# Performance work log

Measured on AMD Instinct MI355X. Metric: run time of the kernel, lower is better.

## Reference

```python
import jax, jax.numpy as jnp
import numpy as np

WS = 8      # window_size
SS = 4      # shift_size
NH = 16     # num_heads


def _rel_position_index(ws):
    # matches WindowMSA.double_step_seq + flip(1)
    seq1 = np.arange(0, (2 * ws - 1) * ws, 2 * ws - 1)
    seq2 = np.arange(0, ws)
    rel = (seq1[:, None] + seq2[None, :]).reshape(1, -1)  # (1, ws*ws)
    idx = rel + rel.T                                      # (ws*ws, ws*ws)
    return np.ascontiguousarray(idx[:, ::-1]).astype(np.int32)


def _shift_attn_mask(H, W, ws, ss):
    # static numpy construction of the Swin shift mask, (nW, N, N)
    img = np.zeros((H, W), dtype=np.int32)
    slices = (slice(0, -ws), slice(-ws, -ss), slice(-ss, None))
    cnt = 0
    for h in slices:
        for w in slices:
            img[h, w] = cnt
            cnt += 1
    win = img.reshape(H // ws, ws, W // ws, ws).transpose(0, 2, 1, 3).reshape(-1, ws * ws)
    diff = win[:, None, :] - win[:, :, None]
    return np.where(diff != 0, -100.0, 0.0).astype(np.float32)


def setup_inputs() -> dict:
    key = jax.random.key(0)
    ks = jax.random.split(key, 6)
    B, H, W, C = 16, 64, 64, 512
    return {
        "query": jax.random.normal(ks[0], (B, H * W, C), jnp.float32),
        "qkv_w": jax.random.normal(ks[1], (3 * C, C), jnp.float32) * 0.02,
        "qkv_b": jnp.zeros((3 * C,), jnp.float32),
        "proj_w": jax.random.normal(ks[2], (C, C), jnp.float32) * 0.02,
        "proj_b": jnp.zeros((C,), jnp.float32),
        "bias_table": jax.random.normal(ks[3], ((2 * WS - 1) ** 2, NH), jnp.float32) * 0.02,
        "rel_index": jnp.asarray(_rel_position_index(WS)),
        "H": H,
        "W": W,
    }


def reference(query, qkv_w, qkv_b, proj_w, proj_b, bias_table, rel_index, H, W):
    B, L, C = query.shape
    hd = C // NH
    scale = hd ** -0.5
    N = WS * WS
    nW = (H // WS) * (W // WS)

    x = query.reshape(B, H, W, C)
    # cyclic shift
    x = jnp.roll(x, (-SS, -SS), axis=(1, 2))
    # window partition -> (B*nW, N, C)
    xw = x.reshape(B, H // WS, WS, W // WS, WS, C).transpose(0, 1, 3, 2, 4, 5)
    xw = xw.reshape(B * nW, N, C)

    # qkv projection
    qkv = xw @ qkv_w.T + qkv_b                       # (BnW, N, 3C)
    qkv = qkv.reshape(B * nW, N, 3, NH, hd).transpose(2, 0, 3, 1, 4)
    q, k, v = qkv[0], qkv[1], qkv[2]                 # (BnW, NH, N, hd)

    attn = jnp.einsum('whnd,whmd->whnm', q * scale, k)

    # relative position bias (N, N, NH) -> (NH, N, N)
    bias = bias_table[rel_index.reshape(-1)].reshape(N, N, NH).transpose(2, 0, 1)
    attn = attn + bias[None]

    # shift mask (static)
    mask = jnp.asarray(_shift_attn_mask(H, W, WS, SS))  # (nW, N, N)
    attn = attn.reshape(B, nW, NH, N, N) + mask[None, :, None]
    attn = jax.nn.softmax(attn.reshape(B * nW, NH, N, N), axis=-1)

    out = jnp.einsum('whnm,whmd->whnd', attn, v)     # (BnW, NH, N, hd)
    out = out.transpose(0, 2, 1, 3).reshape(B * nW, N, C)
    out = out @ proj_w.T + proj_b

    # window reverse -> (B, H, W, C)
    out = out.reshape(B, H // WS, W // WS, WS, WS, C).transpose(0, 1, 3, 2, 4, 5)
    out = out.reshape(B, H, W, C)
    # reverse cyclic shift
    out = jnp.roll(out, (SS, SS), axis=(1, 2))
    return out.reshape(B, H * W, C)
```

## Files before the change

kernel.cpp:

```cpp
#include <hip/hip_runtime.h>


typedef short  short8  __attribute__((ext_vector_type(8)));
typedef short  short4v __attribute__((ext_vector_type(4)));
typedef float  floatx4 __attribute__((ext_vector_type(4)));

#define DEVI static __device__ __forceinline__

DEVI unsigned short f2bf(float f) {
    union { float f; unsigned int u; } v;
    v.f = f;
    return (unsigned short)((v.u + 0x7fffu + ((v.u >> 16) & 1u)) >> 16);
}

__global__ void cvt_all(const float* __restrict__ query,
                        const float* __restrict__ qkv_w,
                        const float* __restrict__ proj_w,
                        unsigned short* __restrict__ wbf,
                        unsigned short* __restrict__ xw) {
    const int bid = blockIdx.x;
    if (bid < 1024) {
        const int idx = ((bid << 8) + threadIdx.x) << 2;
        const float* src = (idx < 786432) ? (qkv_w + idx) : (proj_w + (idx - 786432));
        const floatx4 v = *(const floatx4*)src;
        short4v o;
        o[0] = (short)f2bf(v[0]); o[1] = (short)f2bf(v[1]);
        o[2] = (short)f2bf(v[2]); o[3] = (short)f2bf(v[3]);
        *(short4v*)(wbf + idx) = o;
        return;
    }
    const int c   = ((bid - 1024) << 8) + threadIdx.x;
    const int win = c >> 12;
    const int rem = c & 4095;
    const int jc  = rem & 3;
    const int tok = (rem >> 2) & 63;
    const int kc  = rem >> 8;
    const int b   = win >> 6, wy = (win >> 3) & 7, wx = win & 7;
    const int ty  = tok >> 3, tx = tok & 7;
    const int gh  = ((wy << 3) + ty + 4) & 63;
    const int gw  = ((wx << 3) + tx + 4) & 63;
    const float* src = query + (((b << 12) + (gh << 6) + gw) << 9) + (kc << 5) + (jc << 3);
    const floatx4 v0 = *(const floatx4*)src;
    const floatx4 v1 = *(const floatx4*)(src + 4);
    short8 s;
    s[0] = (short)f2bf(v0[0]); s[1] = (short)f2bf(v0[1]);
    s[2] = (short)f2bf(v0[2]); s[3] = (short)f2bf(v0[3]);
    s[4] = (short)f2bf(v1[0]); s[5] = (short)f2bf(v1[1]);
    s[6] = (short)f2bf(v1[2]); s[7] = (short)f2bf(v1[3]);
    *(short8*)(xw + (win << 15) + (kc << 11) + (tok << 5) + (jc << 3)) = s;
}

template<int GX>
__global__ __launch_bounds__(256, GX ? 2 : 1)
void k_fused(const float* __restrict__ query,
             const unsigned short* __restrict__ wbf,
             const unsigned short* __restrict__ xw,
             const float* __restrict__ qkv_b,
             const float* __restrict__ proj_b,
             const float* __restrict__ bias_table,
             float* __restrict__ out)
{
    __shared__ __align__(16) unsigned short smem[GX ? 33280 : 62976];

    const int tid  = threadIdx.x;
    const int lane = tid & 63;
    const int l15  = lane & 15;
    const int quad = lane >> 4;
    const int wave = tid >> 6;

    const int win = blockIdx.x;
    const int b   = win >> 6;
    const int wy  = (win >> 3) & 7;
    const int wx  = win & 7;
    const int mid = ((wy == 7) ? 2 : 0) | ((wx == 7) ? 1 : 0);

    unsigned short* xs  = smem;
    unsigned short* wb  = smem + (GX ? 0 : 33280) + wave * 7424;
    unsigned short* qbf = wb;
    unsigned short* kbf = wb + 2560;
    unsigned short* vT  = wb + 5120;
    unsigned short* pbf = wb;

    if constexpr (!GX) {
        #pragma unroll
        for (int it = 0; it < 32; ++it) {
            const int c   = tid + (it << 8);
            const int tok = c >> 7;
            const int fo  = (c & 127) << 2;
            const int ty  = tok >> 3, tx = tok & 7;
            const int gh  = ((wy << 3) + ty + 4) & 63;
            const int gw  = ((wx << 3) + tx + 4) & 63;
            const floatx4 v = *(const floatx4*)(query + (((b << 12) + (gh << 6) + gw) << 9) + fo);
            short4v s;
            s[0] = (short)f2bf(v[0]); s[1] = (short)f2bf(v[1]);
            s[2] = (short)f2bf(v[2]); s[3] = (short)f2bf(v[3]);
            *(short4v*)&xs[tok * 520 + fo] = s;
        }
        __syncthreads();
    }

    const unsigned short* xa = xw + (win << 15) + (l15 << 5) + (quad << 3);

    const float scale = 0.17677669529663687f;
    const floatx4 fz = {0.f, 0.f, 0.f, 0.f};

    unsigned int po[4][16];

    for (int hh = 0; hh < 4; ++hh) {
        const int h = (wave << 2) + hh;

        floatx4 accq[4][2], acck[4][2], accv[4][2];
        #pragma unroll
        for (int mt = 0; mt < 4; ++mt)
            #pragma unroll
            for (int nt = 0; nt < 2; ++nt) { accq[mt][nt] = fz; acck[mt][nt] = fz; accv[mt][nt] = fz; }

        const unsigned short* wq = wbf + ((h << 5) + l15) * 512 + (quad << 3);
        const unsigned short* wk = wq + 512 * 512;
        const unsigned short* wv = wk + 512 * 512;

        #pragma unroll 2
        for (int kk = 0; kk < 512; kk += 32) {
            short8 a[4], bq[2], bk2[2], bv2[2];
            #pragma unroll
            for (int mt = 0; mt < 4; ++mt) {
                if constexpr (GX)
                    a[mt] = *(const short8*)(xa + (kk << 6) + (mt << 9));
                else
                    a[mt] = *(const short8*)&xs[((mt << 4) + l15) * 520 + kk + (quad << 3)];
            }
            #pragma unroll
            for (int nt = 0; nt < 2; ++nt) {
                const int ro = (nt << 4) * 512 + kk;
                bq[nt]  = *(const short8*)(wq + ro);
                bk2[nt] = *(const short8*)(wk + ro);
                bv2[nt] = *(const short8*)(wv + ro);
            }
            #pragma unroll
            for (int nt = 0; nt < 2; ++nt)
                #pragma unroll
                for (int mt = 0; mt < 4; ++mt) {
                    accq[mt][nt] = __builtin_amdgcn_mfma_f32_16x16x32_bf16(a[mt], bq[nt],  accq[mt][nt], 0, 0, 0);
                    acck[mt][nt] = __builtin_amdgcn_mfma_f32_16x16x32_bf16(a[mt], bk2[nt], acck[mt][nt], 0, 0, 0);
                    accv[mt][nt] = __builtin_amdgcn_mfma_f32_16x16x32_bf16(a[mt], bv2[nt], accv[mt][nt], 0, 0, 0);
                }
        }

        #pragma unroll
        for (int nt = 0; nt < 2; ++nt) {
            const int cix = (h << 5) + (nt << 4) + l15;
            const float bq_ = qkv_b[cix];
            const float bk_ = qkv_b[512 + cix];
            const float bv_ = qkv_b[1024 + cix];
            #pragma unroll
            for (int mt = 0; mt < 4; ++mt) {
                short4v vv;
                #pragma unroll
                for (int r = 0; r < 4; ++r) {
                    const int row = (mt << 4) + (quad << 2) + r;
                    qbf[row * 40 + (nt << 4) + l15] = f2bf(accq[mt][nt][r] + bq_);
                    kbf[row * 40 + (nt << 4) + l15] = f2bf(acck[mt][nt][r] + bk_);
                    vv[r] = (short)f2bf(accv[mt][nt][r] + bv_);
                }
                *(short4v*)&vT[((nt << 4) + l15) * 72 + (mt << 4) + (quad << 2)] = vv;
            }
        }

        short8 qa[4], ka[4];
        #pragma unroll
        for (int t = 0; t < 4; ++t) {
            qa[t] = *(const short8*)&qbf[((t << 4) + l15) * 40 + (quad << 3)];
            ka[t] = *(const short8*)&kbf[((t << 4) + l15) * 40 + (quad << 3)];
        }
        floatx4 s4[4][4];
        #pragma unroll
        for (int mt = 0; mt < 4; ++mt)
            #pragma unroll
            for (int nt = 0; nt < 4; ++nt)
                s4[mt][nt] = __builtin_amdgcn_mfma_f32_16x16x32_bf16(qa[mt], ka[nt], fz, 0, 0, 0);

        int  gjv[4]; bool jrow[4], jcol[4];
        #pragma unroll
        for (int nt = 0; nt < 4; ++nt) {
            const int j  = (nt << 4) + l15;
            const int j2 = 63 - j;
            gjv[nt]  = 15 * (j2 >> 3) + (j2 & 7);
            jrow[nt] = (j >> 3) < 4;
            jcol[nt] = (j & 7) < 4;
        }
        #pragma unroll
        for (int mt = 0; mt < 4; ++mt) {
            const int i0  = (mt << 4) + (quad << 2);
            const int fi0 = 15 * (i0 >> 3) + (i0 & 7);
            const bool irow = (i0 >> 3) < 4;
            const bool icol = (i0 & 7) == 0;
            #pragma unroll
            for (int nt = 0; nt < 4; ++nt) {
                float mval = 0.0f;
                if ((mid & 2) && (irow != jrow[nt])) mval = -100.0f;
                if ((mid & 1) && (icol != jcol[nt])) mval = -100.0f;
                const float* bp = bias_table + (fi0 + gjv[nt]) * 16 + h;
                #pragma unroll
                for (int r = 0; r < 4; ++r)
                    s4[mt][nt][r] = s4[mt][nt][r] * scale + bp[r * 16] + mval;
            }
        }

        #pragma unroll
        for (int mt = 0; mt < 4; ++mt)
            #pragma unroll
            for (int r = 0; r < 4; ++r) {
                float m = fmaxf(fmaxf(s4[mt][0][r], s4[mt][1][r]),
                                fmaxf(s4[mt][2][r], s4[mt][3][r]));
                m = fmaxf(m, __shfl_xor(m, 1));
                m = fmaxf(m, __shfl_xor(m, 2));
                m = fmaxf(m, __shfl_xor(m, 4));
                m = fmaxf(m, __shfl_xor(m, 8));
                float loc = 0.0f;
                #pragma unroll
                for (int nt = 0; nt < 4; ++nt) {
                    s4[mt][nt][r] = __expf(s4[mt][nt][r] - m);
                    loc += s4[mt][nt][r];
                }
                loc += __shfl_xor(loc, 1);
                loc += __shfl_xor(loc, 2);
                loc += __shfl_xor(loc, 4);
                loc += __shfl_xor(loc, 8);
                const float inv = 1.0f / loc;
                const int row = (mt << 4) + (quad << 2) + r;
                #pragma unroll
                for (int nt = 0; nt < 4; ++nt)
                    pbf[row * 72 + (nt << 4) + l15] = f2bf(s4[mt][nt][r] * inv);
            }

        short8 pa[4][2], va[2][2];
        #pragma unroll
        for (int mt = 0; mt < 4; ++mt)
            #pragma unroll
            for (int ks = 0; ks < 2; ++ks)
                pa[mt][ks] = *(const short8*)&pbf[((mt << 4) + l15) * 72 + (ks << 5) + (quad << 3)];
        #pragma unroll
        for (int nt = 0; nt < 2; ++nt)
            #pragma unroll
            for (int ks = 0; ks < 2; ++ks)
                va[nt][ks] = *(const short8*)&vT[((nt << 4) + l15) * 72 + (ks << 5) + (quad << 3)];

        #pragma unroll
        for (int mt = 0; mt < 4; ++mt)
            #pragma unroll
            for (int nt = 0; nt < 2; ++nt) {
                floatx4 acc = fz;
                acc = __builtin_amdgcn_mfma_f32_16x16x32_bf16(pa[mt][0], va[nt][0], acc, 0, 0, 0);
                acc = __builtin_amdgcn_mfma_f32_16x16x32_bf16(pa[mt][1], va[nt][1], acc, 0, 0, 0);
                const int pi = ((mt << 1) + nt) << 1;
                po[hh][pi]     = (unsigned int)f2bf(acc[0]) | ((unsigned int)f2bf(acc[1]) << 16);
                po[hh][pi + 1] = (unsigned int)f2bf(acc[2]) | ((unsigned int)f2bf(acc[3]) << 16);
            }
    }
    __syncthreads();

    #pragma unroll
    for (int hh = 0; hh < 4; ++hh) {
        const int ch0 = (((wave << 2) + hh) << 5) + l15;
        #pragma unroll
        for (int mt = 0; mt < 4; ++mt)
            #pragma unroll
            for (int nt = 0; nt < 2; ++nt) {
                const int pi = ((mt << 1) + nt) << 1;
                #pragma unroll
                for (int r = 0; r < 4; ++r) {
                    const int row = (mt << 4) + (quad << 2) + r;
                    const unsigned int w = po[hh][pi + (r >> 1)];
                    xs[row * 520 + ch0 + (nt << 4)] =
                        (unsigned short)((w >> ((r & 1) << 4)) & 0xffffu);
                }
            }
    }
    __syncthreads();

    const unsigned short* pwb = wbf + 786432;
    for (int pass = 0; pass < 2; ++pass) {
        const int co0 = (wave << 7) + (pass << 6);
        floatx4 acc[4][4];
        #pragma unroll
        for (int mt = 0; mt < 4; ++mt)
            #pragma unroll
            for (int nt = 0; nt < 4; ++nt) acc[mt][nt] = fz;

        const unsigned short* wp = pwb + (co0 + l15) * 512 + (quad << 3);

        #pragma unroll 2
        for (int kk = 0; kk < 512; kk += 32) {
            short8 a[4], bfr[4];
            #pragma unroll
            for (int mt = 0; mt < 4; ++mt)
                a[mt] = *(const short8*)&xs[((mt << 4) + l15) * 520 + kk + (quad << 3)];
            #pragma unroll
            for (int nt = 0; nt < 4; ++nt)
                bfr[nt] = *(const short8*)(wp + (nt << 4) * 512 + kk);
            #pragma unroll
            for (int nt = 0; nt < 4; ++nt)
                #pragma unroll
                for (int mt = 0; mt < 4; ++mt)
                    acc[mt][nt] = __builtin_amdgcn_mfma_f32_16x16x32_bf16(a[mt], bfr[nt], acc[mt][nt], 0, 0, 0);
        }

        #pragma unroll
        for (int nt = 0; nt < 4; ++nt) {
            const float pb_ = proj_b[co0 + (nt << 4) + l15];
            #pragma unroll
            for (int mt = 0; mt < 4; ++mt)
                #pragma unroll
                for (int r = 0; r < 4; ++r) {
                    const int tok = (mt << 4) + (quad << 2) + r;
                    const int ty = tok >> 3, tx = tok & 7;
                    const int gh = ((wy << 3) + ty + 4) & 63;
                    const int gw = ((wx << 3) + tx + 4) & 63;
                    out[(((b << 12) + (gh << 6) + gw) << 9) + co0 + (nt << 4) + l15] =
                        acc[mt][nt][r] + pb_;
                }
        }
    }
}

extern "C" void kernel_launch(void* const* d_in, const int* in_sizes, int n_in,
                              void* d_out, int out_size, void* d_ws, size_t ws_size,
                              hipStream_t stream) {
    const float* query      = (const float*)d_in[0];
    const float* qkv_w      = (const float*)d_in[1];
    const float* qkv_b      = (const float*)d_in[2];
    const float* proj_w     = (const float*)d_in[3];
    const float* proj_b     = (const float*)d_in[4];
    const float* bias_table = (const float*)d_in[5];

    unsigned short* wbf = (unsigned short*)d_ws;
    unsigned short* xw  = wbf + 1048576;

    const size_t need = (size_t)(1048576 + 33554432) * sizeof(unsigned short);
    if (ws_size >= need) {
        hipLaunchKernelGGL(cvt_all, dim3(17408), dim3(256), 0, stream,
                           query, qkv_w, proj_w, wbf, xw);
        hipLaunchKernelGGL(HIP_KERNEL_NAME(k_fused<1>), dim3(1024), dim3(256), 0, stream,
                           query, wbf, xw, qkv_b, proj_b, bias_table, (float*)d_out);
    } else {
        hipLaunchKernelGGL(cvt_all, dim3(1024), dim3(256), 0, stream,
                           query, qkv_w, proj_w, wbf, wbf);
        hipLaunchKernelGGL(HIP_KERNEL_NAME(k_fused<0>), dim3(1024), dim3(256), 0, stream,
                           query, wbf, wbf, qkv_b, proj_b, bias_table, (float*)d_out);
    }
}
```

Measured before the change: 409.1 us.

## Split fused window attention into separate attention and projection kernels

The fused kernel is split into two. k_attn computes QKV, softmax and PV for each window and writes the bf16 attention output back into the xw buffer in place. k_proj then runs the output projection and un-shifted scatter as its own kernel with higher occupancy. k_attn now uses a smaller, XOR-swizzled per-wave LDS layout so three blocks can fit per CU. The cost is an extra launch plus a bf16 round trip of the attention output through global memory.

```diff
diff --git a/kernel.cpp b/kernel.cpp
--- a/kernel.cpp
+++ b/kernel.cpp
@@ -50,17 +50,13 @@
     *(short8*)(xw + (win << 15) + (kc << 11) + (tok << 5) + (jc << 3)) = s;
 }
 
-template<int GX>
-__global__ __launch_bounds__(256, GX ? 2 : 1)
-void k_fused(const float* __restrict__ query,
-             const unsigned short* __restrict__ wbf,
-             const unsigned short* __restrict__ xw,
-             const float* __restrict__ qkv_b,
-             const float* __restrict__ proj_b,
-             const float* __restrict__ bias_table,
-             float* __restrict__ out)
+__global__ __launch_bounds__(256, 3)
+void k_attn(const unsigned short* __restrict__ wbf,
+            unsigned short* __restrict__ xw,
+            const float* __restrict__ qkv_b,
+            const float* __restrict__ bias_table)
 {
-    __shared__ __align__(16) unsigned short smem[GX ? 33280 : 62976];
+    __shared__ __align__(16) unsigned short smem[24576];
 
     const int tid  = threadIdx.x;
     const int lane = tid & 63;
@@ -69,46 +65,321 @@
     const int wave = tid >> 6;
 
     const int win = blockIdx.x;
+    const int wy  = (win >> 3) & 7;
+    const int wx  = win & 7;
+    const int mid = ((wy == 7) ? 2 : 0) | ((wx == 7) ? 1 : 0);
+
+    unsigned short* wbs = smem + wave * 6144;
+    unsigned short* qbf = wbs;
+    unsigned short* kbf = wbs + 2048;
+    unsigned short* vT  = wbs + 4096;
+    unsigned short* pbf = wbs;
+
+    const int sw4 = (l15 & 3) ^ (l15 >> 2);
+    const int sw8 = (l15 & 7) ^ (l15 >> 3);
+
+    const unsigned short* xa = xw + (win << 15) + (l15 << 5) + (quad << 3);
+
+    const float scale = 0.17677669529663687f;
+    const floatx4 fz = {0.f, 0.f, 0.f, 0.f};
+
+    unsigned int po[4][16];
+
+    for (int hh = 0; hh < 4; ++hh) {
+        const int h = (wave << 2) + hh;
+
+        floatx4 accq[4][2], acck[4][2], accv[4][2];
+        #pragma unroll
+        for (int mt = 0; mt < 4; ++mt)
+            #pragma unroll
+            for (int nt = 0; nt < 2; ++nt) { accq[mt][nt] = fz; acck[mt][nt] = fz; accv[mt][nt] = fz; }
+
+        const unsigned short* wq = wbf + ((h << 5) + l15) * 512 + (quad << 3);
+        const unsigned short* wk = wq + 512 * 512;
+        const unsigned short* wv = wk + 512 * 512;
+
+        #pragma unroll 2
+        for (int kk = 0; kk < 512; kk += 32) {
+            short8 a[4], bq[2], bk2[2], bv2[2];
+            #pragma unroll
+            for (int mt = 0; mt < 4; ++mt)
+                a[mt] = *(const short8*)(xa + (kk << 6) + (mt << 9));
+            #pragma unroll
+            for (int nt = 0; nt < 2; ++nt) {
+                const int ro = (nt << 4) * 512 + kk;
+                bq[nt]  = *(const short8*)(wq + ro);
+                bk2[nt] = *(const short8*)(wk + ro);
+                bv2[nt] = *(const short8*)(wv + ro);
+            }
+            #pragma unroll
+            for (int nt = 0; nt < 2; ++nt)
+                #pragma unroll
+                for (int mt = 0; mt < 4; ++mt) {
+                    accq[mt][nt] = __builtin_amdgcn_mfma_f32_16x16x32_bf16(a[mt], bq[nt],  accq[mt][nt], 0, 0, 0);
+                    acck[mt][nt] = __builtin_amdgcn_mfma_f32_16x16x32_bf16(a[mt], bk2[nt], acck[mt][nt], 0, 0, 0);
+                    accv[mt][nt] = __builtin_amdgcn_mfma_f32_16x16x32_bf16(a[mt], bv2[nt], accv[mt][nt], 0, 0, 0);
+                }
+        }
+
+        #pragma unroll
+        for (int nt = 0; nt < 2; ++nt) {
+            const int cix = (h << 5) + (nt << 4) + l15;
+            const float bq_ = qkv_b[cix];
+            const float bk_ = qkv_b[512 + cix];
+            const float bv_ = qkv_b[1024 + cix];
+            #pragma unroll
+            for (int mt = 0; mt < 4; ++mt) {
+                short4v vv;
+                #pragma unroll
+                for (int r = 0; r < 4; ++r) {
+                    const int row = (mt << 4) + (quad << 2) + r;
+                    const int ph  = (2 * nt + (l15 >> 3)) ^ (row & 3) ^ ((row >> 2) & 3);
+                    const int off = (row << 5) + (l15 & 7) + (ph << 3);
+                    qbf[off] = f2bf(accq[mt][nt][r] + bq_);
+                    kbf[off] = f2bf(acck[mt][nt][r] + bk_);
+                    vv[r] = (short)f2bf(accv[mt][nt][r] + bv_);
+                }
+                const int vph = (2 * mt + (quad >> 1)) ^ sw8;
+                *(short4v*)&vT[(((nt << 4) + l15) << 6) + ((quad & 1) << 2) + (vph << 3)] = vv;
+            }
+        }
+
+        short8 qa[4], ka[4];
+        #pragma unroll
+        for (int t = 0; t < 4; ++t) {
+            const int off = ((((t << 4) + l15)) << 5) + ((quad ^ sw4) << 3);
+            qa[t] = *(const short8*)&qbf[off];
+            ka[t] = *(const short8*)&kbf[off];
+        }
+        floatx4 s4[4][4];
+        #pragma unroll
+        for (int mt = 0; mt < 4; ++mt)
+            #pragma unroll
+            for (int nt = 0; nt < 4; ++nt)
+                s4[mt][nt] = __builtin_amdgcn_mfma_f32_16x16x32_bf16(qa[mt], ka[nt], fz, 0, 0, 0);
+
+        int  gjv[4]; bool jrow[4], jcol[4];
+        #pragma unroll
+        for (int nt = 0; nt < 4; ++nt) {
+            const int j  = (nt << 4) + l15;
+            const int j2 = 63 - j;
+            gjv[nt]  = 15 * (j2 >> 3) + (j2 & 7);
+            jrow[nt] = (j >> 3) < 4;
+            jcol[nt] = (j & 7) < 4;
+        }
+        #pragma unroll
+        for (int mt = 0; mt < 4; ++mt) {
+            const int i0  = (mt << 4) + (quad << 2);
+            const int fi0 = 15 * (i0 >> 3) + (i0 & 7);
+            const bool irow = (i0 >> 3) < 4;
+            const bool icol = (i0 & 7) == 0;
+            #pragma unroll
+            for (int nt = 0; nt < 4; ++nt) {
+                float mval = 0.0f;
+                if ((mid & 2) && (irow != jrow[nt])) mval = -100.0f;
+                if ((mid & 1) && (icol != jcol[nt])) mval = -100.0f;
+                const float* bp = bias_table + (fi0 + gjv[nt]) * 16 + h;
+                #pragma unroll
+                for (int r = 0; r < 4; ++r)
+                    s4[mt][nt][r] = s4[mt][nt][r] * scale + bp[r * 16] + mval;
+            }
+        }
+
+        float linv[4][4];
+        #pragma unroll
+        for (int mt = 0; mt < 4; ++mt)
+            #pragma unroll
+            for (int r = 0; r < 4; ++r) {
+                float m = fmaxf(fmaxf(s4[mt][0][r], s4[mt][1][r]),
+                                fmaxf(s4[mt][2][r], s4[mt][3][r]));
+                m = fmaxf(m, __shfl_xor(m, 1));
+                m = fmaxf(m, __shfl_xor(m, 2));
+                m = fmaxf(m, __shfl_xor(m, 4));
+                m = fmaxf(m, __shfl_xor(m, 8));
+                float loc = 0.0f;
+                #pragma unroll
+                for (int nt = 0; nt < 4; ++nt) {
+                    s4[mt][nt][r] = __expf(s4[mt][nt][r] - m);
+                    loc += s4[mt][nt][r];
+                }
+                loc += __shfl_xor(loc, 1);
+                loc += __shfl_xor(loc, 2);
+                loc += __shfl_xor(loc, 4);
+                loc += __shfl_xor(loc, 8);
+                linv[mt][r] = 1.0f / loc;
+                const int row = (mt << 4) + (quad << 2) + r;
+                #pragma unroll
+                for (int nt = 0; nt < 4; ++nt) {
+                    const int ph = (2 * nt + (l15 >> 3)) ^ (row & 7) ^ ((row >> 3) & 1);
+                    pbf[(row << 6) + (l15 & 7) + (ph << 3)] = f2bf(s4[mt][nt][r]);
+                }
+            }
+
+        short8 pa[4][2], va[2][2];
+        #pragma unroll
+        for (int mt = 0; mt < 4; ++mt)
+            #pragma unroll
+            for (int ks = 0; ks < 2; ++ks)
+                pa[mt][ks] = *(const short8*)&pbf[((((mt << 4) + l15)) << 6) + ((((ks << 2) + quad) ^ sw8) << 3)];
+        #pragma unroll
+        for (int nt = 0; nt < 2; ++nt)
+            #pragma unroll
+            for (int ks = 0; ks < 2; ++ks)
+                va[nt][ks] = *(const short8*)&vT[((((nt << 4) + l15)) << 6) + ((((ks << 2) + quad) ^ sw8) << 3)];
+
+        #pragma unroll
+        for (int mt = 0; mt < 4; ++mt)
+            #pragma unroll
+            for (int nt = 0; nt < 2; ++nt) {
+                floatx4 acc = fz;
+                acc = __builtin_amdgcn_mfma_f32_16x16x32_bf16(pa[mt][0], va[nt][0], acc, 0, 0, 0);
+                acc = __builtin_amdgcn_mfma_f32_16x16x32_bf16(pa[mt][1], va[nt][1], acc, 0, 0, 0);
+                const int pi = ((mt << 1) + nt) << 1;
+                po[hh][pi]     = (unsigned int)f2bf(acc[0] * linv[mt][0]) |
+                                 ((unsigned int)f2bf(acc[1] * linv[mt][1]) << 16);
+                po[hh][pi + 1] = (unsigned int)f2bf(acc[2] * linv[mt][2]) |
+                                 ((unsigned int)f2bf(acc[3] * linv[mt][3]) << 16);
+            }
+    }
+
+    __syncthreads();
+
+    unsigned short* yw = xw + (win << 15);
+    #pragma unroll
+    for (int hh = 0; hh < 4; ++hh) {
+        const int kcb = ((wave << 2) + hh) << 11;
+        #pragma unroll
+        for (int mt = 0; mt < 4; ++mt)
+            #pragma unroll
+            for (int nt = 0; nt < 2; ++nt) {
+                const int pi = ((mt << 1) + nt) << 1;
+                #pragma unroll
+                for (int r = 0; r < 4; ++r) {
+                    const int tok = (mt << 4) + (quad << 2) + r;
+                    const unsigned int w = po[hh][pi + (r >> 1)];
+                    yw[kcb + (tok << 5) + (nt << 4) + l15] =
+                        (unsigned short)((w >> ((r & 1) << 4)) & 0xffffu);
+                }
+            }
+    }
+}
+
+__global__ __launch_bounds__(256, 4)
+void k_proj(const unsigned short* __restrict__ wbf,
+            const unsigned short* __restrict__ yw,
+            const float* __restrict__ proj_b,
+            float* __restrict__ out)
+{
+    const int tid  = threadIdx.x;
+    const int lane = tid & 63;
+    const int l15  = lane & 15;
+    const int quad = lane >> 4;
+    const int wave = tid >> 6;
+
+    const int win = blockIdx.x;
+    const int b   = win >> 6;
+    const int wy  = (win >> 3) & 7;
+    const int wx  = win & 7;
+
+    const unsigned short* ya  = yw + (win << 15) + (l15 << 5) + (quad << 3);
+    const unsigned short* pwb = wbf + 786432;
+    const floatx4 fz = {0.f, 0.f, 0.f, 0.f};
+
+    for (int pass = 0; pass < 2; ++pass) {
+        const int co0 = (wave << 7) + (pass << 6);
+        floatx4 acc[4][4];
+        #pragma unroll
+        for (int mt = 0; mt < 4; ++mt)
+            #pragma unroll
+            for (int nt = 0; nt < 4; ++nt) acc[mt][nt] = fz;
+
+        const unsigned short* wp = pwb + (co0 + l15) * 512 + (quad << 3);
+
+        #pragma unroll 2
+        for (int kk = 0; kk < 512; kk += 32) {
+            short8 a[4], bfr[4];
+            #pragma unroll
+            for (int mt = 0; mt < 4; ++mt)
+                a[mt] = *(const short8*)(ya + (kk << 6) + (mt << 9));
+            #pragma unroll
+            for (int nt = 0; nt < 4; ++nt)
+                bfr[nt] = *(const short8*)(wp + (nt << 4) * 512 + kk);
+            #pragma unroll
+            for (int nt = 0; nt < 4; ++nt)
+                #pragma unroll
+                for (int mt = 0; mt < 4; ++mt)
+                    acc[mt][nt] = __builtin_amdgcn_mfma_f32_16x16x32_bf16(a[mt], bfr[nt], acc[mt][nt], 0, 0, 0);
+        }
+
+        #pragma unroll
+        for (int nt = 0; nt < 4; ++nt) {
+            const float pb_ = proj_b[co0 + (nt << 4) + l15];
+            #pragma unroll
+            for (int mt = 0; mt < 4; ++mt)
+                #pragma unroll
+                for (int r = 0; r < 4; ++r) {
+                    const int tok = (mt << 4) + (quad << 2) + r;
+                    const int ty = tok >> 3, tx = tok & 7;
+                    const int gh = ((wy << 3) + ty + 4) & 63;
+                    const int gw = ((wx << 3) + tx + 4) & 63;
+                    out[(((b << 12) + (gh << 6) + gw) << 9) + co0 + (nt << 4) + l15] =
+                        acc[mt][nt][r] + pb_;
+                }
+        }
+    }
+}
+
+__global__ __launch_bounds__(256, 1)
+void k_legacy(const float* __restrict__ query,
+              const unsigned short* __restrict__ wbf,
+              const float* __restrict__ qkv_b,
+              const float* __restrict__ proj_b,
+              const float* __restrict__ bias_table,
+              float* __restrict__ out)
+{
+    __shared__ __align__(16) unsigned short smem[62976];
+
+    const int tid  = threadIdx.x;
+    const int lane = tid & 63;
+    const int l15  = lane & 15;
+    const int quad = lane >> 4;
+    const int wave = tid >> 6;
+
+    const int win = blockIdx.x;
     const int b   = win >> 6;
     const int wy  = (win >> 3) & 7;
     const int wx  = win & 7;
     const int mid = ((wy == 7) ? 2 : 0) | ((wx == 7) ? 1 : 0);
 
     unsigned short* xs  = smem;
-    unsigned short* wb  = smem + (GX ? 0 : 33280) + wave * 7424;
+    unsigned short* wb  = smem + 33280 + wave * 7424;
     unsigned short* qbf = wb;
     unsigned short* kbf = wb + 2560;
     unsigned short* vT  = wb + 5120;
     unsigned short* pbf = wb;
 
-    if constexpr (!GX) {
-        #pragma unroll
-        for (int it = 0; it < 32; ++it) {
-            const int c   = tid + (it << 8);
-            const int tok = c >> 7;
-            const int fo  = (c & 127) << 2;
-            const int ty  = tok >> 3, tx = tok & 7;
-            const int gh  = ((wy << 3) + ty + 4) & 63;
-            const int gw  = ((wx << 3) + tx + 4) & 63;
-            const floatx4 v = *(const floatx4*)(query + (((b << 12) + (gh << 6) + gw) << 9) + fo);
-            short4v s;
-            s[0] = (short)f2bf(v[0]); s[1] = (short)f2bf(v[1]);
-            s[2] = (short)f2bf(v[2]); s[3] = (short)f2bf(v[3]);
-            *(short4v*)&xs[tok * 520 + fo] = s;
-        }
-        __syncthreads();
-    }
-
-    const unsigned short* xa = xw + (win << 15) + (l15 << 5) + (quad << 3);
+    #pragma unroll
+    for (int it = 0; it < 32; ++it) {
+        const int c   = tid + (it << 8);
+        const int tok = c >> 7;
+        const int fo  = (c & 127) << 2;
+        const int ty  = tok >> 3, tx = tok & 7;
+        const int gh  = ((wy << 3) + ty + 4) & 63;
+        const int gw  = ((wx << 3) + tx + 4) & 63;
+        const floatx4 v = *(const floatx4*)(query + (((b << 12) + (gh << 6) + gw) << 9) + fo);
+        short4v s;
+        s[0] = (short)f2bf(v[0]); s[1] = (short)f2bf(v[1]);
+        s[2] = (short)f2bf(v[2]); s[3] = (short)f2bf(v[3]);
+        *(short4v*)&xs[tok * 520 + fo] = s;
+    }
+    __syncthreads();
 
     const float scale = 0.17677669529663687f;
     const floatx4 fz = {0.f, 0.f, 0.f, 0.f};
-
     unsigned int po[4][16];
 
     for (int hh = 0; hh < 4; ++hh) {
         const int h = (wave << 2) + hh;
-
         floatx4 accq[4][2], acck[4][2], accv[4][2];
         #pragma unroll
         for (int mt = 0; mt < 4; ++mt)
@@ -123,12 +394,8 @@
         for (int kk = 0; kk < 512; kk += 32) {
             short8 a[4], bq[2], bk2[2], bv2[2];
             #pragma unroll
-            for (int mt = 0; mt < 4; ++mt) {
-                if constexpr (GX)
-                    a[mt] = *(const short8*)(xa + (kk << 6) + (mt << 9));
-                else
-                    a[mt] = *(const short8*)&xs[((mt << 4) + l15) * 520 + kk + (quad << 3)];
-            }
+            for (int mt = 0; mt < 4; ++mt)
+                a[mt] = *(const short8*)&xs[((mt << 4) + l15) * 520 + kk + (quad << 3)];
             #pragma unroll
             for (int nt = 0; nt < 2; ++nt) {
                 const int ro = (nt << 4) * 512 + kk;
@@ -340,12 +607,14 @@
     if (ws_size >= need) {
         hipLaunchKernelGGL(cvt_all, dim3(17408), dim3(256), 0, stream,
                            query, qkv_w, proj_w, wbf, xw);
-        hipLaunchKernelGGL(HIP_KERNEL_NAME(k_fused<1>), dim3(1024), dim3(256), 0, stream,
-                           query, wbf, xw, qkv_b, proj_b, bias_table, (float*)d_out);
+        hipLaunchKernelGGL(k_attn, dim3(1024), dim3(256), 0, stream,
+                           wbf, xw, qkv_b, bias_table);
+        hipLaunchKernelGGL(k_proj, dim3(1024), dim3(256), 0, stream,
+                           wbf, xw, proj_b, (float*)d_out);
     } else {
         hipLaunchKernelGGL(cvt_all, dim3(1024), dim3(256), 0, stream,
                            query, qkv_w, proj_w, wbf, wbf);
-        hipLaunchKernelGGL(HIP_KERNEL_NAME(k_fused<0>), dim3(1024), dim3(256), 0, stream,
-                           query, wbf, wbf, qkv_b, proj_b, bias_table, (float*)d_out);
+        hipLaunchKernelGGL(k_legacy, dim3(1024), dim3(256), 0, stream,
+                           query, wbf, qkv_b, proj_b, bias_table, (float*)d_out);
     }
 }
```

Measured after the change: 876.7 us. +114.3%, slower.
